# Kernel optimization log

Measured on AMD Instinct MI355X. Metric: run time of the kernel, lower is better.

## Reference

```python
import jax, jax.numpy as jnp
import numpy as np

D_MODEL = 2048
NUM_TILES = 64
D_SLICE = D_MODEL // NUM_TILES  # 32
TILES_PER_CLUSTER = 8
NUM_CLUSTERS = NUM_TILES // TILES_PER_CLUSTER  # 8
GRID = 16
LN_EPS = 1e-5

# per-tile owned dimension indices: (tile_id*d_slice + j) % d_model  -> disjoint contiguous slices
DIMS = (np.arange(NUM_TILES)[:, None] * D_SLICE + np.arange(D_SLICE)[None, :]) % D_MODEL  # [T, d_slice]
DIMS = jnp.asarray(DIMS, dtype=jnp.int32)


def setup_inputs() -> dict:
    key = jax.random.key(0)
    k1, k2, k3, k4, k5, k6 = jax.random.split(key, 6)
    x = jax.random.normal(k1, (4, 4096, D_MODEL), dtype=jnp.float32)
    ln_gamma = 1.0 + 0.1 * jax.random.normal(k2, (D_MODEL,), dtype=jnp.float32)
    ln_beta = 0.1 * jax.random.normal(k3, (D_MODEL,), dtype=jnp.float32)
    spline_bases = 0.1 * jax.random.normal(k4, (NUM_TILES, D_SLICE, GRID), dtype=jnp.float32)
    spline_slopes = 0.1 + 0.1 * jax.random.normal(k5, (NUM_TILES, D_SLICE, GRID), dtype=jnp.float32)
    output_scale = 1.0 + 0.1 * jax.random.normal(k6, (NUM_TILES,), dtype=jnp.float32)
    return {"x": x, "ln_gamma": ln_gamma, "ln_beta": ln_beta,
            "spline_bases": spline_bases, "spline_slopes": spline_slopes,
            "output_scale": output_scale}


def _forward(x, ln_gamma, ln_beta, spline_bases, spline_slopes, output_scale):
    B, S, D = x.shape
    N = B * S
    # --- input LayerNorm (eval mode, dropout is identity) ---
    mu = jnp.mean(x, axis=-1, keepdims=True)
    var = jnp.mean(jnp.square(x - mu), axis=-1, keepdims=True)
    xn = (x - mu) * jax.lax.rsqrt(var + LN_EPS) * ln_gamma + ln_beta
    xf = xn.reshape(N, D)

    # --- tile / cluster signatures (hierarchy built from fresh EMA = current sigs) ---
    slope_sign = jnp.sign(jnp.mean(spline_slopes, axis=-1))           # [T, d_slice]
    tile_sigs = jnp.zeros((NUM_TILES, D), dtype=x.dtype)
    tile_sigs = tile_sigs.at[jnp.arange(NUM_TILES)[:, None], DIMS].set(slope_sign)  # [T, D]
    cluster_sigs = jnp.sign(tile_sigs.reshape(NUM_CLUSTERS, TILES_PER_CLUSTER, D).mean(axis=1))  # [C, D]
    cluster_assign = jnp.arange(NUM_TILES, dtype=jnp.int32) // TILES_PER_CLUSTER  # [T]

    # --- two-level routing ---
    input_sigs = jnp.sign(xf)                                          # [N, D]
    cluster_scores = input_sigs @ cluster_sigs.T                       # [N, C]
    best_cluster = jnp.argmax(cluster_scores, axis=-1)                 # [N]
    tile_scores = input_sigs @ tile_sigs.T                             # [N, T]
    in_cluster = cluster_assign[None, :] == best_cluster[:, None]      # [N, T]
    tile_idx = jnp.argmax(jnp.where(in_cluster, tile_scores, -jnp.inf), axis=-1)  # [N]

    # --- per-tile KAN spline evaluation on owned slice ---
    tok_dims = DIMS[tile_idx]                                          # [N, d_slice]
    x_slice = jnp.take_along_axis(xf, tok_dims, axis=1)                # [N, d_slice]
    # per-tile scalar min/max over all routed tokens and slice dims (matches x_slice.min()/.max())
    tok_min = x_slice.min(axis=1)                                      # [N]
    tok_max = x_slice.max(axis=1)
    onehot = tile_idx[None, :] == jnp.arange(NUM_TILES)[:, None]       # [T, N]
    tile_min = jnp.where(onehot, tok_min[None, :], jnp.inf).min(axis=1)    # [T]
    tile_max = jnp.where(onehot, tok_max[None, :], -jnp.inf).max(axis=1)   # [T]
    mn = tile_min[tile_idx][:, None]
    mx = tile_max[tile_idx][:, None]
    u = jnp.clip((x_slice - mn) / (mx - mn + 1e-8), 0.0, 1.0 - 1e-6)   # [N, d_slice]
    gi = jnp.clip((u * GRID).astype(jnp.int32), 0, GRID - 1)           # [N, d_slice]
    j = jnp.arange(D_SLICE)[None, :]
    b = spline_bases[tile_idx[:, None], j, gi]                         # [N, d_slice]
    s = spline_slopes[tile_idx[:, None], j, gi]
    x_local = (u - gi.astype(u.dtype) / GRID) * GRID
    delta = (b + s * x_local) * output_scale[tile_idx][:, None]        # [N, d_slice]

    # --- scatter delta into tile's slice (tile use_residual=False -> zeros elsewhere) ---
    out = jnp.zeros_like(xf).at[jnp.arange(N)[:, None], tok_dims].set(delta)
    # FFN residual bus
    return x + out.reshape(B, S, D)


def reference(x, ln_gamma, ln_beta, spline_bases, spline_slopes, output_scale):
    return _forward(x, ln_gamma, ln_beta, spline_bases, spline_slopes, output_scale)
```

## Files before the change

### kernel.cpp

```cpp
#include <hip/hip_runtime.h>

#define D_MODEL 2048
#define NUM_TILES 64
#define D_SLICE 32
#define TILES_PER_CLUSTER 8
#define NUM_CLUSTERS 8
#define GRID_PTS 16
#define LN_EPS 1e-5f
#define NBUCKET 64

__device__ __forceinline__ unsigned int encF(float f) {
    unsigned int u = __float_as_uint(f);
    return (u & 0x80000000u) ? ~u : (u | 0x80000000u);
}
__device__ __forceinline__ float decF(unsigned int u) {
    unsigned int b = (u & 0x80000000u) ? (u ^ 0x80000000u) : ~u;
    return __uint_as_float(b);
}

__global__ void kan_setup(const float* __restrict__ slopes,
                          float* __restrict__ sgn,
                          unsigned int* __restrict__ tminb,
                          unsigned int* __restrict__ tmaxb) {
    int d = blockIdx.x * blockDim.x + threadIdx.x;
    if (d < NUM_TILES * NBUCKET) { tminb[d] = 0xFFFFFFFFu; tmaxb[d] = 0u; }
    if (d < D_MODEL) {
        const float* p = slopes + (size_t)d * GRID_PTS;
        float s = 0.f;
#pragma unroll
        for (int k = 0; k < GRID_PTS; ++k) s += p[k];
        float m = s * (1.0f / GRID_PTS);
        sgn[d] = (m > 0.f) ? 1.f : ((m < 0.f) ? -1.f : 0.f);
    }
}

__launch_bounds__(256)
__global__ void kan_main(const float* __restrict__ x,
                         const float* __restrict__ gamma,
                         const float* __restrict__ beta,
                         const float* __restrict__ sgn,
                         float* __restrict__ out,
                         float* __restrict__ xn_slice,
                         int* __restrict__ tidx_out,
                         unsigned int* __restrict__ tminb,
                         unsigned int* __restrict__ tmaxb) {
    const int n = blockIdx.x;
    const int tid = threadIdx.x;
    const size_t base = (size_t)n * D_MODEL + (size_t)tid * 8;

    float4 a = *(const float4*)(x + base);
    float4 b = *(const float4*)(x + base + 4);
    float xv[8] = {a.x, a.y, a.z, a.w, b.x, b.y, b.z, b.w};

    __shared__ float red[4];
    __shared__ int ts[NUM_TILES];
    __shared__ int cs[NUM_CLUSTERS];
    __shared__ int chosen;

    float s = 0.f;
#pragma unroll
    for (int k = 0; k < 8; ++k) s += xv[k];
#pragma unroll
    for (int off = 32; off > 0; off >>= 1) s += __shfl_down(s, off);
    if ((tid & 63) == 0) red[tid >> 6] = s;
    __syncthreads();
    float mu = (red[0] + red[1] + red[2] + red[3]) * (1.0f / D_MODEL);
    __syncthreads();

    float s2 = 0.f;
#pragma unroll
    for (int k = 0; k < 8; ++k) { float dvt = xv[k] - mu; s2 += dvt * dvt; }
#pragma unroll
    for (int off = 32; off > 0; off >>= 1) s2 += __shfl_down(s2, off);
    if ((tid & 63) == 0) red[tid >> 6] = s2;
    __syncthreads();
    float var = (red[0] + red[1] + red[2] + red[3]) * (1.0f / D_MODEL);
    float rs = rsqrtf(var + LN_EPS);

    float4 g0 = *(const float4*)(gamma + tid * 8);
    float4 g1 = *(const float4*)(gamma + tid * 8 + 4);
    float4 b0 = *(const float4*)(beta + tid * 8);
    float4 b1 = *(const float4*)(beta + tid * 8 + 4);
    float4 sg0 = *(const float4*)(sgn + tid * 8);
    float4 sg1 = *(const float4*)(sgn + tid * 8 + 4);
    float gv[8] = {g0.x, g0.y, g0.z, g0.w, g1.x, g1.y, g1.z, g1.w};
    float bv[8] = {b0.x, b0.y, b0.z, b0.w, b1.x, b1.y, b1.z, b1.w};
    float sv[8] = {sg0.x, sg0.y, sg0.z, sg0.w, sg1.x, sg1.y, sg1.z, sg1.w};

    float xn[8];
    int sc = 0;
#pragma unroll
    for (int k = 0; k < 8; ++k) {
        xn[k] = (xv[k] - mu) * rs * gv[k] + bv[k];
        int s1 = (xn[k] > 0.f) ? 1 : ((xn[k] < 0.f) ? -1 : 0);
        sc += s1 * (int)sv[k];
    }
    sc += __shfl_xor(sc, 1);
    sc += __shfl_xor(sc, 2);
    if ((tid & 3) == 0) ts[tid >> 2] = sc;
    __syncthreads();

    if (tid < NUM_CLUSTERS) {
        int c = 0;
#pragma unroll
        for (int t = 0; t < TILES_PER_CLUSTER; ++t) c += ts[tid * TILES_PER_CLUSTER + t];
        cs[tid] = c;
    }
    __syncthreads();
    if (tid == 0) {
        int bc = 0, bv_ = -2147483647;
#pragma unroll
        for (int c = 0; c < NUM_CLUSTERS; ++c)
            if (cs[c] > bv_) { bv_ = cs[c]; bc = c; }
        int t0 = bc * TILES_PER_CLUSTER;
        int bt = t0, btv = ts[t0];
#pragma unroll
        for (int t = 1; t < TILES_PER_CLUSTER; ++t)
            if (ts[t0 + t] > btv) { btv = ts[t0 + t]; bt = t0 + t; }
        chosen = bt;
        tidx_out[n] = bt;
    }
    __syncthreads();
    int tile = chosen;

    *(float4*)(out + base) = a;
    *(float4*)(out + base + 4) = b;

    if ((tid >> 2) == tile) {
        float* q = xn_slice + (size_t)n * D_SLICE + (tid & 3) * 8;
        *(float4*)(q) = make_float4(xn[0], xn[1], xn[2], xn[3]);
        *(float4*)(q + 4) = make_float4(xn[4], xn[5], xn[6], xn[7]);
    }

    float mn8 = xn[0], mx8 = xn[0];
#pragma unroll
    for (int k = 1; k < 8; ++k) { mn8 = fminf(mn8, xn[k]); mx8 = fmaxf(mx8, xn[k]); }
    mn8 = fminf(mn8, __shfl_xor(mn8, 1));
    mn8 = fminf(mn8, __shfl_xor(mn8, 2));
    mx8 = fmaxf(mx8, __shfl_xor(mx8, 1));
    mx8 = fmaxf(mx8, __shfl_xor(mx8, 2));
    if (tid == tile * 4) {
        int bkt = blockIdx.x & (NBUCKET - 1);
        atomicMin(&tminb[tile * NBUCKET + bkt], encF(mn8));
        atomicMax(&tmaxb[tile * NBUCKET + bkt], encF(mx8));
    }
}

__global__ void kan_reduce(const unsigned int* __restrict__ tminb,
                           const unsigned int* __restrict__ tmaxb,
                           unsigned int* __restrict__ tmin,
                           unsigned int* __restrict__ tmax) {
    int t = threadIdx.x;
    unsigned int mn = 0xFFFFFFFFu, mx = 0u;
#pragma unroll 4
    for (int b = 0; b < NBUCKET; ++b) {
        mn = min(mn, tminb[t * NBUCKET + b]);
        mx = max(mx, tmaxb[t * NBUCKET + b]);
    }
    tmin[t] = mn;
    tmax[t] = mx;
}

__global__ void kan_apply(const float* __restrict__ xn_slice,
                          const int* __restrict__ tidx,
                          const float* __restrict__ bases,
                          const float* __restrict__ slopes,
                          const float* __restrict__ oscale,
                          const unsigned int* __restrict__ tmin,
                          const unsigned int* __restrict__ tmax,
                          float* __restrict__ out, int N) {
    int g = blockIdx.x * blockDim.x + threadIdx.x;
    if (g >= N * D_SLICE) return;
    int n = g >> 5;
    int j = g & 31;
    int t = tidx[n];
    float xnv = xn_slice[g];
    float mn = decF(tmin[t]);
    float mx = decF(tmax[t]);
    float u = (xnv - mn) / (mx - mn + 1e-8f);
    u = fminf(fmaxf(u, 0.0f), 1.0f - 1e-6f);
    int gi = (int)(u * (float)GRID_PTS);
    gi = min(max(gi, 0), GRID_PTS - 1);
    int off = (t * D_SLICE + j) * GRID_PTS + gi;
    float bb = bases[off];
    float ss = slopes[off];
    float xl = (u - (float)gi * (1.0f / GRID_PTS)) * (float)GRID_PTS;
    float delta = (bb + ss * xl) * oscale[t];
    size_t oi = (size_t)n * D_MODEL + t * D_SLICE + j;
    out[oi] = out[oi] + delta;
}

extern "C" void kernel_launch(void* const* d_in, const int* in_sizes, int n_in,
                              void* d_out, int out_size, void* d_ws, size_t ws_size,
                              hipStream_t stream) {
    const float* x      = (const float*)d_in[0];
    const float* gamma  = (const float*)d_in[1];
    const float* beta   = (const float*)d_in[2];
    const float* bases  = (const float*)d_in[3];
    const float* slopes = (const float*)d_in[4];
    const float* oscale = (const float*)d_in[5];
    float* out = (float*)d_out;
    const int N = in_sizes[0] / D_MODEL;

    char* w = (char*)d_ws;
    unsigned int* tminb = (unsigned int*)w; w += NUM_TILES * NBUCKET * 4;
    unsigned int* tmaxb = (unsigned int*)w; w += NUM_TILES * NBUCKET * 4;
    unsigned int* tmin  = (unsigned int*)w; w += 256;
    unsigned int* tmax  = (unsigned int*)w; w += 256;
    float* sgn = (float*)w;  w += D_MODEL * sizeof(float);
    int* tidx = (int*)w;     w += (size_t)N * sizeof(int);
    float* xns = (float*)w;  w += (size_t)N * D_SLICE * sizeof(float);

    kan_setup<<<(NUM_TILES * NBUCKET + 255) / 256, 256, 0, stream>>>(slopes, sgn, tminb, tmaxb);
    kan_main<<<N, 256, 0, stream>>>(x, gamma, beta, sgn, out, xns, tidx, tminb, tmaxb);
    kan_reduce<<<1, 64, 0, stream>>>(tminb, tmaxb, tmin, tmax);
    kan_apply<<<(N * D_SLICE + 255) / 256, 256, 0, stream>>>(xns, tidx, bases, slopes,
                                                             oscale, tmin, tmax, out, N);
}
```

Measured before the change: 65.75 us.

## Process one token per wavefront and route with shuffles, no LDS

The main kernel now gives each 64-lane wavefront one token row (four rows per block) in place of one row per 256-thread block. LayerNorm statistics and the tile/cluster score reductions use only cross-lane shuffles, which removes the shared-memory staging and the five block-level barriers. Column mapping changes to strided float4 chunks so each 8-lane group covers one tile's slice, and tile selection uses a packed max key. The cost is more registers per thread and an assumption that N is divisible by 4.

Result: slower. 133.0 us (+102.2%).

```diff
diff --git a/kernel.cpp b/kernel.cpp
--- a/kernel.cpp
+++ b/kernel.cpp
@@ -33,6 +33,11 @@
         sgn[d] = (m > 0.f) ? 1.f : ((m < 0.f) ? -1.f : 0.f);
     }
 }
+
+#define SEL8(dst, idx, A)                                              \
+    dst = (idx == 0) ? A[0] : (idx == 1) ? A[1] : (idx == 2) ? A[2] :  \
+          (idx == 3) ? A[3] : (idx == 4) ? A[4] : (idx == 5) ? A[5] :  \
+          (idx == 6) ? A[6] : A[7];
 
 __launch_bounds__(256)
 __global__ void kan_main(const float* __restrict__ x,
@@ -44,106 +49,113 @@
                          int* __restrict__ tidx_out,
                          unsigned int* __restrict__ tminb,
                          unsigned int* __restrict__ tmaxb) {
-    const int n = blockIdx.x;
-    const int tid = threadIdx.x;
-    const size_t base = (size_t)n * D_MODEL + (size_t)tid * 8;
-
-    float4 a = *(const float4*)(x + base);
-    float4 b = *(const float4*)(x + base + 4);
-    float xv[8] = {a.x, a.y, a.z, a.w, b.x, b.y, b.z, b.w};
-
-    __shared__ float red[4];
-    __shared__ int ts[NUM_TILES];
-    __shared__ int cs[NUM_CLUSTERS];
-    __shared__ int chosen;
+    const int wid = threadIdx.x >> 6;
+    const int l   = threadIdx.x & 63;
+    const int n   = blockIdx.x * 4 + wid;
+    const size_t rowb = (size_t)n * D_MODEL;
+
+    const float* xr = x + rowb + 4 * l;
+    float4 xv[8];
+#pragma unroll
+    for (int c = 0; c < 8; ++c) xv[c] = *(const float4*)(xr + 256 * c);
 
     float s = 0.f;
 #pragma unroll
-    for (int k = 0; k < 8; ++k) s += xv[k];
-#pragma unroll
-    for (int off = 32; off > 0; off >>= 1) s += __shfl_down(s, off);
-    if ((tid & 63) == 0) red[tid >> 6] = s;
-    __syncthreads();
-    float mu = (red[0] + red[1] + red[2] + red[3]) * (1.0f / D_MODEL);
-    __syncthreads();
-
-    float s2 = 0.f;
-#pragma unroll
-    for (int k = 0; k < 8; ++k) { float dvt = xv[k] - mu; s2 += dvt * dvt; }
-#pragma unroll
-    for (int off = 32; off > 0; off >>= 1) s2 += __shfl_down(s2, off);
-    if ((tid & 63) == 0) red[tid >> 6] = s2;
-    __syncthreads();
-    float var = (red[0] + red[1] + red[2] + red[3]) * (1.0f / D_MODEL);
-    float rs = rsqrtf(var + LN_EPS);
-
-    float4 g0 = *(const float4*)(gamma + tid * 8);
-    float4 g1 = *(const float4*)(gamma + tid * 8 + 4);
-    float4 b0 = *(const float4*)(beta + tid * 8);
-    float4 b1 = *(const float4*)(beta + tid * 8 + 4);
-    float4 sg0 = *(const float4*)(sgn + tid * 8);
-    float4 sg1 = *(const float4*)(sgn + tid * 8 + 4);
-    float gv[8] = {g0.x, g0.y, g0.z, g0.w, g1.x, g1.y, g1.z, g1.w};
-    float bv[8] = {b0.x, b0.y, b0.z, b0.w, b1.x, b1.y, b1.z, b1.w};
-    float sv[8] = {sg0.x, sg0.y, sg0.z, sg0.w, sg1.x, sg1.y, sg1.z, sg1.w};
-
-    float xn[8];
-    int sc = 0;
-#pragma unroll
-    for (int k = 0; k < 8; ++k) {
-        xn[k] = (xv[k] - mu) * rs * gv[k] + bv[k];
-        int s1 = (xn[k] > 0.f) ? 1 : ((xn[k] < 0.f) ? -1 : 0);
-        sc += s1 * (int)sv[k];
-    }
-    sc += __shfl_xor(sc, 1);
-    sc += __shfl_xor(sc, 2);
-    if ((tid & 3) == 0) ts[tid >> 2] = sc;
-    __syncthreads();
-
-    if (tid < NUM_CLUSTERS) {
-        int c = 0;
-#pragma unroll
-        for (int t = 0; t < TILES_PER_CLUSTER; ++t) c += ts[tid * TILES_PER_CLUSTER + t];
-        cs[tid] = c;
-    }
-    __syncthreads();
-    if (tid == 0) {
-        int bc = 0, bv_ = -2147483647;
-#pragma unroll
-        for (int c = 0; c < NUM_CLUSTERS; ++c)
-            if (cs[c] > bv_) { bv_ = cs[c]; bc = c; }
-        int t0 = bc * TILES_PER_CLUSTER;
-        int bt = t0, btv = ts[t0];
-#pragma unroll
-        for (int t = 1; t < TILES_PER_CLUSTER; ++t)
-            if (ts[t0 + t] > btv) { btv = ts[t0 + t]; bt = t0 + t; }
-        chosen = bt;
-        tidx_out[n] = bt;
-    }
-    __syncthreads();
-    int tile = chosen;
-
-    *(float4*)(out + base) = a;
-    *(float4*)(out + base + 4) = b;
-
-    if ((tid >> 2) == tile) {
-        float* q = xn_slice + (size_t)n * D_SLICE + (tid & 3) * 8;
-        *(float4*)(q) = make_float4(xn[0], xn[1], xn[2], xn[3]);
-        *(float4*)(q + 4) = make_float4(xn[4], xn[5], xn[6], xn[7]);
-    }
-
-    float mn8 = xn[0], mx8 = xn[0];
-#pragma unroll
-    for (int k = 1; k < 8; ++k) { mn8 = fminf(mn8, xn[k]); mx8 = fmaxf(mx8, xn[k]); }
-    mn8 = fminf(mn8, __shfl_xor(mn8, 1));
-    mn8 = fminf(mn8, __shfl_xor(mn8, 2));
-    mx8 = fmaxf(mx8, __shfl_xor(mx8, 1));
-    mx8 = fmaxf(mx8, __shfl_xor(mx8, 2));
-    if (tid == tile * 4) {
-        int bkt = blockIdx.x & (NBUCKET - 1);
-        atomicMin(&tminb[tile * NBUCKET + bkt], encF(mn8));
-        atomicMax(&tmaxb[tile * NBUCKET + bkt], encF(mx8));
-    }
+    for (int c = 0; c < 8; ++c) s += xv[c].x + xv[c].y + xv[c].z + xv[c].w;
+#pragma unroll
+    for (int off = 32; off > 0; off >>= 1) s += __shfl_xor(s, off);
+    const float mu = s * (1.0f / D_MODEL);
+
+    float v = 0.f;
+#pragma unroll
+    for (int c = 0; c < 8; ++c) {
+        float dx = xv[c].x - mu, dy = xv[c].y - mu, dz = xv[c].z - mu, dw = xv[c].w - mu;
+        v += dx * dx + dy * dy + dz * dz + dw * dw;
+    }
+#pragma unroll
+    for (int off = 32; off > 0; off >>= 1) v += __shfl_xor(v, off);
+    const float rs = rsqrtf(v * (1.0f / D_MODEL) + LN_EPS);
+
+    float* orow = out + rowb + 4 * l;
+#pragma unroll
+    for (int c = 0; c < 8; ++c) *(float4*)(orow + 256 * c) = xv[c];
+
+    const float* gr = gamma + 4 * l;
+    const float* br = beta + 4 * l;
+    const float* sr = sgn + 4 * l;
+    int ts[8];
+#pragma unroll
+    for (int c = 0; c < 8; ++c) {
+        float4 g  = *(const float4*)(gr + 256 * c);
+        float4 bb = *(const float4*)(br + 256 * c);
+        float4 sg = *(const float4*)(sr + 256 * c);
+        float n0 = (xv[c].x - mu) * rs * g.x + bb.x;
+        float n1 = (xv[c].y - mu) * rs * g.y + bb.y;
+        float n2 = (xv[c].z - mu) * rs * g.z + bb.z;
+        float n3 = (xv[c].w - mu) * rs * g.w + bb.w;
+        int sc = 0;
+        sc += ((n0 > 0.f) - (n0 < 0.f)) * (int)sg.x;
+        sc += ((n1 > 0.f) - (n1 < 0.f)) * (int)sg.y;
+        sc += ((n2 > 0.f) - (n2 < 0.f)) * (int)sg.z;
+        sc += ((n3 > 0.f) - (n3 < 0.f)) * (int)sg.w;
+        sc += __shfl_xor(sc, 1);
+        sc += __shfl_xor(sc, 2);
+        sc += __shfl_xor(sc, 4);
+        ts[c] = sc;
+    }
+
+    int cs[8];
+#pragma unroll
+    for (int c = 0; c < 8; ++c) {
+        int t = ts[c];
+        t += __shfl_xor(t, 8);
+        t += __shfl_xor(t, 16);
+        t += __shfl_xor(t, 32);
+        cs[c] = t;
+    }
+
+    int bc = 0, bv = cs[0];
+#pragma unroll
+    for (int c = 1; c < 8; ++c)
+        if (cs[c] > bv) { bv = cs[c]; bc = c; }
+
+    int tsv;
+    SEL8(tsv, bc, ts);
+    const int k = l >> 3;
+    int key = ((tsv + 64) << 3) | (7 - k);
+    key = max(key, __shfl_xor(key, 8));
+    key = max(key, __shfl_xor(key, 16));
+    key = max(key, __shfl_xor(key, 32));
+    const int kwin = 7 - (key & 7);
+    const int tile = bc * 8 + kwin;
+
+    float4 xs;
+    SEL8(xs, bc, xv);
+    float4 g  = *(const float4*)(gamma + 256 * bc + 4 * l);
+    float4 bb = *(const float4*)(beta  + 256 * bc + 4 * l);
+    float4 xn4;
+    xn4.x = (xs.x - mu) * rs * g.x + bb.x;
+    xn4.y = (xs.y - mu) * rs * g.y + bb.y;
+    xn4.z = (xs.z - mu) * rs * g.z + bb.z;
+    xn4.w = (xs.w - mu) * rs * g.w + bb.w;
+
+    if (k == kwin)
+        *(float4*)(xn_slice + (size_t)n * D_SLICE + 4 * (l & 7)) = xn4;
+
+    float mn = fminf(fminf(xn4.x, xn4.y), fminf(xn4.z, xn4.w));
+    float mx = fmaxf(fmaxf(xn4.x, xn4.y), fmaxf(xn4.z, xn4.w));
+    mn = fminf(mn, __shfl_xor(mn, 1));
+    mn = fminf(mn, __shfl_xor(mn, 2));
+    mn = fminf(mn, __shfl_xor(mn, 4));
+    mx = fmaxf(mx, __shfl_xor(mx, 1));
+    mx = fmaxf(mx, __shfl_xor(mx, 2));
+    mx = fmaxf(mx, __shfl_xor(mx, 4));
+    if (l == kwin * 8) {
+        int bkt = n & (NBUCKET - 1);
+        atomicMin(&tminb[tile * NBUCKET + bkt], encF(mn));
+        atomicMax(&tmaxb[tile * NBUCKET + bkt], encF(mx));
+    }
+    if (l == 0) tidx_out[n] = tile;
 }
 
 __global__ void kan_reduce(const unsigned int* __restrict__ tminb,
@@ -212,7 +224,7 @@
     float* xns = (float*)w;  w += (size_t)N * D_SLICE * sizeof(float);
 
     kan_setup<<<(NUM_TILES * NBUCKET + 255) / 256, 256, 0, stream>>>(slopes, sgn, tminb, tmaxb);
-    kan_main<<<N, 256, 0, stream>>>(x, gamma, beta, sgn, out, xns, tidx, tminb, tmaxb);
+    kan_main<<<N / 4, 256, 0, stream>>>(x, gamma, beta, sgn, out, xns, tidx, tminb, tmaxb);
     kan_reduce<<<1, 64, 0, stream>>>(tminb, tmaxb, tmin, tmax);
     kan_apply<<<(N * D_SLICE + 255) / 256, 256, 0, stream>>>(xns, tidx, bases, slopes,
                                                              oscale, tmin, tmax, out, N);
```

## Fuse LayerNorm reductions, store output early non-temporally, vectorize spline apply

Applied to the files above, without the earlier changes.

The LayerNorm mean and variance are now computed in one pass as sum and sum of squares, which removes one reduction round and its barriers. The copy of x to the output is issued right after the load using non-temporal stores, and the gamma, beta and sign loads are hoisted ahead of the reduction so their latency overlaps it. The apply kernel now handles four elements per thread with vector loads and stores, and uses one reciprocal instead of a division per element. Single-pass variance is less numerically stable, and non-temporal stores may evict the output lines that kan_apply later reads back.

After: 63.15 us. 1.04x faster.

```diff
diff --git a/kernel.cpp b/kernel.cpp
--- a/kernel.cpp
+++ b/kernel.cpp
@@ -8,6 +8,8 @@
 #define GRID_PTS 16
 #define LN_EPS 1e-5f
 #define NBUCKET 64
+
+typedef float f32x4 __attribute__((ext_vector_type(4)));
 
 __device__ __forceinline__ unsigned int encF(float f) {
     unsigned int u = __float_as_uint(f);
@@ -48,41 +50,43 @@
     const int tid = threadIdx.x;
     const size_t base = (size_t)n * D_MODEL + (size_t)tid * 8;
 
-    float4 a = *(const float4*)(x + base);
-    float4 b = *(const float4*)(x + base + 4);
+    f32x4 a = *(const f32x4*)(x + base);
+    f32x4 b = *(const f32x4*)(x + base + 4);
+
+    __builtin_nontemporal_store(a, (f32x4*)(out + base));
+    __builtin_nontemporal_store(b, (f32x4*)(out + base + 4));
+
+    f32x4 g0 = *(const f32x4*)(gamma + tid * 8);
+    f32x4 g1 = *(const f32x4*)(gamma + tid * 8 + 4);
+    f32x4 b0 = *(const f32x4*)(beta + tid * 8);
+    f32x4 b1 = *(const f32x4*)(beta + tid * 8 + 4);
+    f32x4 sg0 = *(const f32x4*)(sgn + tid * 8);
+    f32x4 sg1 = *(const f32x4*)(sgn + tid * 8 + 4);
+
     float xv[8] = {a.x, a.y, a.z, a.w, b.x, b.y, b.z, b.w};
 
-    __shared__ float red[4];
+    __shared__ float2 red[4];
     __shared__ int ts[NUM_TILES];
     __shared__ int cs[NUM_CLUSTERS];
     __shared__ int chosen;
 
-    float s = 0.f;
-#pragma unroll
-    for (int k = 0; k < 8; ++k) s += xv[k];
-#pragma unroll
-    for (int off = 32; off > 0; off >>= 1) s += __shfl_down(s, off);
-    if ((tid & 63) == 0) red[tid >> 6] = s;
-    __syncthreads();
-    float mu = (red[0] + red[1] + red[2] + red[3]) * (1.0f / D_MODEL);
-    __syncthreads();
-
-    float s2 = 0.f;
-#pragma unroll
-    for (int k = 0; k < 8; ++k) { float dvt = xv[k] - mu; s2 += dvt * dvt; }
-#pragma unroll
-    for (int off = 32; off > 0; off >>= 1) s2 += __shfl_down(s2, off);
-    if ((tid & 63) == 0) red[tid >> 6] = s2;
-    __syncthreads();
-    float var = (red[0] + red[1] + red[2] + red[3]) * (1.0f / D_MODEL);
-    float rs = rsqrtf(var + LN_EPS);
-
-    float4 g0 = *(const float4*)(gamma + tid * 8);
-    float4 g1 = *(const float4*)(gamma + tid * 8 + 4);
-    float4 b0 = *(const float4*)(beta + tid * 8);
-    float4 b1 = *(const float4*)(beta + tid * 8 + 4);
-    float4 sg0 = *(const float4*)(sgn + tid * 8);
-    float4 sg1 = *(const float4*)(sgn + tid * 8 + 4);
+    float s = 0.f, q = 0.f;
+#pragma unroll
+    for (int k = 0; k < 8; ++k) { s += xv[k]; q += xv[k] * xv[k]; }
+#pragma unroll
+    for (int off = 32; off > 0; off >>= 1) {
+        s += __shfl_xor(s, off);
+        q += __shfl_xor(q, off);
+    }
+    if ((tid & 63) == 0) red[tid >> 6] = make_float2(s, q);
+    __syncthreads();
+    float S = red[0].x + red[1].x + red[2].x + red[3].x;
+    float Q = red[0].y + red[1].y + red[2].y + red[3].y;
+    const float mu = S * (1.0f / D_MODEL);
+    float var = Q * (1.0f / D_MODEL) - mu * mu;
+    var = fmaxf(var, 0.0f);
+    const float rs = rsqrtf(var + LN_EPS);
+
     float gv[8] = {g0.x, g0.y, g0.z, g0.w, g1.x, g1.y, g1.z, g1.w};
     float bv[8] = {b0.x, b0.y, b0.z, b0.w, b1.x, b1.y, b1.z, b1.w};
     float sv[8] = {sg0.x, sg0.y, sg0.z, sg0.w, sg1.x, sg1.y, sg1.z, sg1.w};
@@ -121,15 +125,12 @@
         tidx_out[n] = bt;
     }
     __syncthreads();
-    int tile = chosen;
-
-    *(float4*)(out + base) = a;
-    *(float4*)(out + base + 4) = b;
+    const int tile = chosen;
 
     if ((tid >> 2) == tile) {
-        float* q = xn_slice + (size_t)n * D_SLICE + (tid & 3) * 8;
-        *(float4*)(q) = make_float4(xn[0], xn[1], xn[2], xn[3]);
-        *(float4*)(q + 4) = make_float4(xn[4], xn[5], xn[6], xn[7]);
+        float* qp = xn_slice + (size_t)n * D_SLICE + (tid & 3) * 8;
+        *(f32x4*)(qp) = f32x4{xn[0], xn[1], xn[2], xn[3]};
+        *(f32x4*)(qp + 4) = f32x4{xn[4], xn[5], xn[6], xn[7]};
     }
 
     float mn8 = xn[0], mx8 = xn[0];
@@ -170,24 +171,33 @@
                           const unsigned int* __restrict__ tmax,
                           float* __restrict__ out, int N) {
     int g = blockIdx.x * blockDim.x + threadIdx.x;
-    if (g >= N * D_SLICE) return;
-    int n = g >> 5;
-    int j = g & 31;
+    if (g >= N * 8) return;
+    int n = g >> 3;
+    int qd = g & 7;
     int t = tidx[n];
-    float xnv = xn_slice[g];
+    f32x4 xn4 = *(const f32x4*)(xn_slice + (size_t)n * D_SLICE + qd * 4);
     float mn = decF(tmin[t]);
     float mx = decF(tmax[t]);
-    float u = (xnv - mn) / (mx - mn + 1e-8f);
-    u = fminf(fmaxf(u, 0.0f), 1.0f - 1e-6f);
-    int gi = (int)(u * (float)GRID_PTS);
-    gi = min(max(gi, 0), GRID_PTS - 1);
-    int off = (t * D_SLICE + j) * GRID_PTS + gi;
-    float bb = bases[off];
-    float ss = slopes[off];
-    float xl = (u - (float)gi * (1.0f / GRID_PTS)) * (float)GRID_PTS;
-    float delta = (bb + ss * xl) * oscale[t];
-    size_t oi = (size_t)n * D_MODEL + t * D_SLICE + j;
-    out[oi] = out[oi] + delta;
+    float inv = 1.0f / (mx - mn + 1e-8f);
+    float osc = oscale[t];
+
+    float dl[4];
+    float xnv[4] = {xn4.x, xn4.y, xn4.z, xn4.w};
+#pragma unroll
+    for (int e = 0; e < 4; ++e) {
+        float u = (xnv[e] - mn) * inv;
+        u = fminf(fmaxf(u, 0.0f), 1.0f - 1e-6f);
+        int gi = (int)(u * (float)GRID_PTS);
+        gi = min(max(gi, 0), GRID_PTS - 1);
+        int j = qd * 4 + e;
+        int off = (t * D_SLICE + j) * GRID_PTS + gi;
+        float xl = (u - (float)gi * (1.0f / GRID_PTS)) * (float)GRID_PTS;
+        dl[e] = (bases[off] + slopes[off] * xl) * osc;
+    }
+    size_t oi = (size_t)n * D_MODEL + t * D_SLICE + qd * 4;
+    f32x4 o = *(f32x4*)(out + oi);
+    o.x += dl[0]; o.y += dl[1]; o.z += dl[2]; o.w += dl[3];
+    *(f32x4*)(out + oi) = o;
 }
 
 extern "C" void kernel_launch(void* const* d_in, const int* in_sizes, int n_in,
@@ -214,6 +224,6 @@
     kan_setup<<<(NUM_TILES * NBUCKET + 255) / 256, 256, 0, stream>>>(slopes, sgn, tminb, tmaxb);
     kan_main<<<N, 256, 0, stream>>>(x, gamma, beta, sgn, out, xns, tidx, tminb, tmaxb);
     kan_reduce<<<1, 64, 0, stream>>>(tminb, tmaxb, tmin, tmax);
-    kan_apply<<<(N * D_SLICE + 255) / 256, 256, 0, stream>>>(xns, tidx, bases, slopes,
-                                                             oscale, tmin, tmax, out, N);
-}
+    kan_apply<<<(N * 8 + 255) / 256, 256, 0, stream>>>(xns, tidx, bases, slopes,
+                                                       oscale, tmin, tmax, out, N);
+}
```
